# Kernel tuning notes

Measured on AMD Instinct MI355X. Metric: run time of the kernel, lower is better.

Reference implementation:

```python
import jax, jax.numpy as jnp
import numpy as np

N_NODES = 50000
N_EDGES = 800000
C_IN = 128
C_OUT = 64
C_HID = 2 * C_OUT  # 128


def setup_inputs() -> dict:
    key = jax.random.key(0)
    ks = jax.random.split(key, 8)
    x = jax.random.normal(ks[0], (N_NODES, C_IN), dtype=jnp.float32)
    edge_index = jax.random.randint(ks[1], (2, N_EDGES), 0, N_NODES, dtype=jnp.int64)
    s1 = 1.0 / np.sqrt(C_IN)
    s2 = 1.0 / np.sqrt(C_HID)
    s3 = 1.0 / np.sqrt(C_OUT)
    W1 = jax.random.uniform(ks[2], (C_IN, C_HID), jnp.float32, -s1, s1)
    b1 = jnp.zeros((C_HID,), jnp.float32)
    W2 = jax.random.uniform(ks[3], (C_HID, C_OUT), jnp.float32, -s2, s2)
    b2 = jnp.zeros((C_OUT,), jnp.float32)
    Wb = jax.random.uniform(ks[4], (1, C_OUT, C_OUT), jnp.float32, -s3, s3)
    bb = jax.random.uniform(ks[5], (1,), jnp.float32, -s3, s3)
    return {"x": x, "edge_index": edge_index, "W1": W1, "b1": b1,
            "W2": W2, "b2": b2, "Wb": Wb, "bb": bb}


def gcn_conv(x, W, b, src, dst, n_nodes):
    # PyG GCNConv: h = x @ W; add self-loops; symmetric normalization D^-1/2 (A+I) D^-1/2.
    h = x @ W  # [N, F]
    ones = jnp.ones((src.shape[0],), h.dtype)
    deg = jax.ops.segment_sum(ones, dst, num_segments=n_nodes) + 1.0  # +1 for self-loop
    dinv = jax.lax.rsqrt(deg)
    norm = dinv[src] * dinv[dst]  # [E]
    msgs = h[src] * norm[:, None]  # [E, F]
    agg = jax.ops.segment_sum(msgs, dst, num_segments=n_nodes)
    # self-loop contribution: norm_ii = 1/deg_i
    agg = agg + h * (1.0 / deg)[:, None]
    return agg + b


def reference(x, edge_index, W1, b1, W2, b2, Wb, bb):
    src = edge_index[0]
    dst = edge_index[1]
    n = x.shape[0]
    # encode
    h = jax.nn.relu(gcn_conv(x, W1, b1, src, dst, n))
    z = gcn_conv(h, W2, b2, src, dst, n)  # [N, C_OUT]
    # decode: bilinear on (z[src], z[dst]) -> sigmoid
    zs = z[src]  # [E, C_OUT]
    zd = z[dst]  # [E, C_OUT]
    logits = jnp.einsum('ec,ocd,ed->eo', zs, Wb, zd) + bb  # [E, 1]
    return jax.nn.sigmoid(logits)
```

## Files before the change

### kernel.cpp

```cpp
#include <hip/hip_runtime.h>
#include <hip/hip_bf16.h>


#define N_NODES 50000
#define BSH 7
#define BSZ 128
#define NBUCK ((N_NODES + BSZ - 1) / BSZ)
#define EPB 4096
#define CAP 3072
#define DSPLIT 4

typedef unsigned int u32;
typedef unsigned short u16;
typedef unsigned long long u64;

typedef __attribute__((ext_vector_type(8))) short bf16x8;
typedef __attribute__((ext_vector_type(4))) float f32x4;
union frag_u { bf16x8 f; u32 u[4]; uint4 v; };

__device__ __forceinline__ float bflo(u32 u) { return __uint_as_float(u << 16); }
__device__ __forceinline__ float bfhi(u32 u) { return __uint_as_float(u & 0xffff0000u); }
__device__ __forceinline__ u32 f2bf(float f) {
    u32 b = __float_as_uint(f);
    return (b + 0x7fffu + ((b >> 16) & 1u)) >> 16;
}
__device__ __forceinline__ u32 pack2(float a, float b) { return f2bf(a) | (f2bf(b) << 16); }

__global__ __launch_bounds__(256) void gemm1_scatter(
        const float* __restrict__ X, const float* __restrict__ W,
        u16* __restrict__ O, int n_rows, int gblk,
        const int* __restrict__ src, const int* __restrict__ dst,
        int* __restrict__ bcur, u64* __restrict__ pair, int E) {
    constexpr int K = 128, NOUT = 128;
    constexpr int KP = K + 8;
    constexpr int NT = NOUT / 16;
    constexpr int KS = K / 32;
    __shared__ __align__(16) char smem[NOUT * KP * 2 * sizeof(u16)];
    int t = threadIdx.x;

    if ((int)blockIdx.x < gblk) {
        u16* Wt_hi = (u16*)smem;
        u16* Wt_lo = Wt_hi + NOUT * KP;
        for (int i4 = t; i4 < K * NOUT / 4; i4 += 256) {
            int k = (i4 * 4) / NOUT;
            int n0 = (i4 * 4) % NOUT;
            float4 w4 = *(const float4*)&W[(size_t)k * NOUT + n0];
            float wv[4] = {w4.x, w4.y, w4.z, w4.w};
#pragma unroll
            for (int q = 0; q < 4; q++) {
                u32 hi = f2bf(wv[q]);
                u32 lo = f2bf(wv[q] - bflo(hi));
                Wt_hi[(n0 + q) * KP + k] = (u16)hi;
                Wt_lo[(n0 + q) * KP + k] = (u16)lo;
            }
        }
        __syncthreads();

        int wave = t >> 6;
        int lane = t & 63;
        int m16 = lane & 15;
        int quad = lane >> 4;
        int row0 = blockIdx.x * 128 + wave * 32;

        f32x4 acc[2][NT] = {};
        for (int ks = 0; ks < KS; ks++) {
            frag_u a_hi[2], a_lo[2];
#pragma unroll
            for (int mt = 0; mt < 2; mt++) {
                int row = row0 + mt * 16 + m16;
                row = row < n_rows ? row : n_rows - 1;
                const float* Xp = X + (size_t)row * K + ks * 32 + quad * 8;
                float4 x0 = *(const float4*)Xp;
                float4 x1 = *(const float4*)(Xp + 4);
                float xv[8] = {x0.x, x0.y, x0.z, x0.w, x1.x, x1.y, x1.z, x1.w};
#pragma unroll
                for (int p = 0; p < 4; p++) {
                    u32 h0 = f2bf(xv[2 * p]), h1 = f2bf(xv[2 * p + 1]);
                    a_hi[mt].u[p] = h0 | (h1 << 16);
                    a_lo[mt].u[p] = pack2(xv[2 * p] - bflo(h0), xv[2 * p + 1] - bflo(h1));
                }
            }
#pragma unroll
            for (int nt = 0; nt < NT; nt++) {
                int n = nt * 16 + m16;
                frag_u b_hi, b_lo;
                b_hi.v = *(const uint4*)&Wt_hi[n * KP + ks * 32 + quad * 8];
                b_lo.v = *(const uint4*)&Wt_lo[n * KP + ks * 32 + quad * 8];
#pragma unroll
                for (int mt = 0; mt < 2; mt++) {
                    acc[mt][nt] = __builtin_amdgcn_mfma_f32_16x16x32_bf16(a_hi[mt].f, b_hi.f, acc[mt][nt], 0, 0, 0);
                    acc[mt][nt] = __builtin_amdgcn_mfma_f32_16x16x32_bf16(a_hi[mt].f, b_lo.f, acc[mt][nt], 0, 0, 0);
                    acc[mt][nt] = __builtin_amdgcn_mfma_f32_16x16x32_bf16(a_lo[mt].f, b_hi.f, acc[mt][nt], 0, 0, 0);
                }
            }
        }
#pragma unroll
        for (int mt = 0; mt < 2; mt++)
#pragma unroll
            for (int nt = 0; nt < NT; nt++)
#pragma unroll
                for (int r = 0; r < 4; r++) {
                    int row = row0 + mt * 16 + quad * 4 + r;
                    if (row < n_rows)
                        O[(size_t)row * NOUT + nt * 16 + m16] = (u16)f2bf(acc[mt][nt][r]);
                }
    } else {
        int* hist = (int*)smem;
        for (int i = t; i < NBUCK; i += 256) hist[i] = 0;
        __syncthreads();
        int base = ((int)blockIdx.x - gblk) * EPB;
        int s_[16], d_[16];
#pragma unroll
        for (int it = 0; it < 16; it++) {
            int e = base + it * 256 + t;
            if (e < E) {
                s_[it] = src[e];
                d_[it] = dst[e];
                atomicAdd(&hist[d_[it] >> BSH], 1);
            } else {
                d_[it] = -1;
            }
        }
        __syncthreads();
        for (int b = t; b < NBUCK; b += 256) {
            int c = hist[b];
            hist[b] = c ? (b * CAP + atomicAdd(&bcur[b], c)) : 0;
        }
        __syncthreads();
#pragma unroll
        for (int it = 0; it < 16; it++) {
            if (d_[it] >= 0) {
                int b = d_[it] >> BSH;
                int off = atomicAdd(&hist[b], 1);
                int e = base + it * 256 + t;
                pair[off] = (u64)((u32)s_[it] | ((u32)(d_[it] & (BSZ - 1)) << 16))
                          | ((u64)(u32)e << 32);
            }
        }
    }
}

__global__ __launch_bounds__(256) void bucket_sort(const u64* __restrict__ pair,
                                                   const int* __restrict__ bcur,
                                                   int* __restrict__ row_ptr,
                                                   int* __restrict__ col,
                                                   u32* __restrict__ eidx,
                                                   float* __restrict__ dinv,
                                                   float* __restrict__ inv, int n, int E) {
    __shared__ int ssum[256];
    __shared__ int cnt[BSZ];
    __shared__ int scn[BSZ];
    __shared__ int cur[BSZ];
    int t = threadIdx.x;
    int base = blockIdx.x << BSH;
    int nn = min(BSZ, n - base);
    int accp = 0;
    for (int i = t; i < (int)blockIdx.x; i += 256) accp += bcur[i];
    ssum[t] = accp;
    __syncthreads();
    for (int s = 128; s > 0; s >>= 1) {
        if (t < s) ssum[t] += ssum[t + s];
        __syncthreads();
    }
    int b0 = ssum[0];
    int cntE = bcur[blockIdx.x];
    int p0 = blockIdx.x * CAP;
    if (t < BSZ) cnt[t] = 0;
    __syncthreads();
    for (int j = t; j < cntE; j += 256)
        atomicAdd(&cnt[(int)((pair[p0 + j] >> 16) & (BSZ - 1))], 1);
    __syncthreads();
    if (t < BSZ) scn[t] = cnt[t];
    __syncthreads();
    for (int off = 1; off < BSZ; off <<= 1) {
        int a = (t < BSZ && t >= off) ? scn[t - off] : 0;
        __syncthreads();
        if (t < BSZ) scn[t] += a;
        __syncthreads();
    }
    if (t < nn) {
        int excl = b0 + scn[t] - cnt[t];
        row_ptr[base + t] = excl;
        cur[t] = excl;
        float d = (float)cnt[t] + 1.0f;
        dinv[base + t] = rsqrtf(d);
        inv[base + t] = 1.0f / d;
    }
    if (t == 0 && blockIdx.x == NBUCK - 1) row_ptr[n] = E;
    __syncthreads();
    for (int j = t; j < cntE; j += 256) {
        u64 p = pair[p0 + j];
        int ln = (int)((p >> 16) & (BSZ - 1));
        int pos = atomicAdd(&cur[ln], 1);
        col[pos] = (int)(p & 0xffffu);
        eidx[pos] = (u32)(p >> 32) | ((u32)ln << 20);
    }
}

template <int K, int NOUT, bool TRANSW>
__global__ __launch_bounds__(256) void gemm_mfma_bf(const u16* __restrict__ Xv,
                                                    const float* __restrict__ W,
                                                    u16* __restrict__ O, int n_rows) {
    constexpr int KP = K + 8;
    constexpr int NT = NOUT / 16;
    constexpr int KS = K / 32;
    __shared__ __align__(16) u16 Wt_hi[NOUT * KP];
    __shared__ __align__(16) u16 Wt_lo[NOUT * KP];
    int t = threadIdx.x;
    for (int i4 = t; i4 < K * NOUT / 4; i4 += 256) {
        if constexpr (!TRANSW) {
            int k = (i4 * 4) / NOUT;
            int n0 = (i4 * 4) % NOUT;
            float4 w4 = *(const float4*)&W[(size_t)k * NOUT + n0];
            float wv[4] = {w4.x, w4.y, w4.z, w4.w};
#pragma unroll
            for (int q = 0; q < 4; q++) {
                u32 hi = f2bf(wv[q]);
                u32 lo = f2bf(wv[q] - bflo(hi));
                Wt_hi[(n0 + q) * KP + k] = (u16)hi;
                Wt_lo[(n0 + q) * KP + k] = (u16)lo;
            }
        } else {
            int n = (i4 * 4) / K;
            int k0 = (i4 * 4) % K;
            float4 w4 = *(const float4*)&W[(size_t)n * K + k0];
            float wv[4] = {w4.x, w4.y, w4.z, w4.w};
#pragma unroll
            for (int q = 0; q < 4; q++) {
                u32 hi = f2bf(wv[q]);
                u32 lo = f2bf(wv[q] - bflo(hi));
                Wt_hi[n * KP + k0 + q] = (u16)hi;
                Wt_lo[n * KP + k0 + q] = (u16)lo;
            }
        }
    }
    __syncthreads();

    int wave = t >> 6;
    int lane = t & 63;
    int m16 = lane & 15;
    int quad = lane >> 4;
    int row0 = blockIdx.x * 128 + wave * 32;

    f32x4 acc[2][NT] = {};
    for (int ks = 0; ks < KS; ks++) {
        frag_u a_hi[2];
#pragma unroll
        for (int mt = 0; mt < 2; mt++) {
            int row = row0 + mt * 16 + m16;
            row = row < n_rows ? row : n_rows - 1;
            a_hi[mt].v = *(const uint4*)(Xv + (size_t)row * K + ks * 32 + quad * 8);
        }
#pragma unroll
        for (int nt = 0; nt < NT; nt++) {
            int n = nt * 16 + m16;
            frag_u b_hi, b_lo;
            b_hi.v = *(const uint4*)&Wt_hi[n * KP + ks * 32 + quad * 8];
            b_lo.v = *(const uint4*)&Wt_lo[n * KP + ks * 32 + quad * 8];
#pragma unroll
            for (int mt = 0; mt < 2; mt++) {
                acc[mt][nt] = __builtin_amdgcn_mfma_f32_16x16x32_bf16(a_hi[mt].f, b_hi.f, acc[mt][nt], 0, 0, 0);
                acc[mt][nt] = __builtin_amdgcn_mfma_f32_16x16x32_bf16(a_hi[mt].f, b_lo.f, acc[mt][nt], 0, 0, 0);
            }
        }
    }
#pragma unroll
    for (int mt = 0; mt < 2; mt++)
#pragma unroll
        for (int nt = 0; nt < NT; nt++)
#pragma unroll
            for (int r = 0; r < 4; r++) {
                int row = row0 + mt * 16 + quad * 4 + r;
                if (row < n_rows)
                    O[(size_t)row * NOUT + nt * 16 + m16] = (u16)f2bf(acc[mt][nt][r]);
            }
}

template <int C, bool RELU>
__global__ __launch_bounds__(256) void agg_pull(const u16* __restrict__ H,
                                                const int* __restrict__ row_ptr,
                                                const int* __restrict__ col,
                                                const float* __restrict__ dinv,
                                                const float* __restrict__ inv,
                                                const float* __restrict__ b,
                                                u16* __restrict__ O, int n) {
    constexpr int TPN = C / 8;
    const uint4* Hv = (const uint4*)H;
    int tid = blockIdx.x * 256 + threadIdx.x;
    int node = tid / TPN;
    if (node >= n) return;
    int part = tid % TPN;
    int c8 = part * 8;
    float dn = dinv[node];
    float iv = inv[node];
    float acc[8];
    {
        uint4 h = Hv[(size_t)node * TPN + part];
        acc[0] = bflo(h.x) * iv + b[c8 + 0];
        acc[1] = bfhi(h.x) * iv + b[c8 + 1];
        acc[2] = bflo(h.y) * iv + b[c8 + 2];
        acc[3] = bfhi(h.y) * iv + b[c8 + 3];
        acc[4] = bflo(h.z) * iv + b[c8 + 4];
        acc[5] = bfhi(h.z) * iv + b[c8 + 5];
        acc[6] = bflo(h.w) * iv + b[c8 + 6];
        acc[7] = bfhi(h.w) * iv + b[c8 + 7];
    }
    int j = row_ptr[node];
    int end = row_ptr[node + 1];
    for (; j + 3 < end; j += 4) {
        int s0 = col[j], s1 = col[j + 1], s2 = col[j + 2], s3 = col[j + 3];
        float n0 = dn * dinv[s0], n1 = dn * dinv[s1];
        float n2 = dn * dinv[s2], n3 = dn * dinv[s3];
        uint4 v0 = Hv[(size_t)s0 * TPN + part];
        uint4 v1 = Hv[(size_t)s1 * TPN + part];
        uint4 v2 = Hv[(size_t)s2 * TPN + part];
        uint4 v3 = Hv[(size_t)s3 * TPN + part];
        acc[0] += bflo(v0.x) * n0 + bflo(v1.x) * n1 + bflo(v2.x) * n2 + bflo(v3.x) * n3;
        acc[1] += bfhi(v0.x) * n0 + bfhi(v1.x) * n1 + bfhi(v2.x) * n2 + bfhi(v3.x) * n3;
        acc[2] += bflo(v0.y) * n0 + bflo(v1.y) * n1 + bflo(v2.y) * n2 + bflo(v3.y) * n3;
        acc[3] += bfhi(v0.y) * n0 + bfhi(v1.y) * n1 + bfhi(v2.y) * n2 + bfhi(v3.y) * n3;
        acc[4] += bflo(v0.z) * n0 + bflo(v1.z) * n1 + bflo(v2.z) * n2 + bflo(v3.z) * n3;
        acc[5] += bfhi(v0.z) * n0 + bfhi(v1.z) * n1 + bfhi(v2.z) * n2 + bfhi(v3.z) * n3;
        acc[6] += bflo(v0.w) * n0 + bflo(v1.w) * n1 + bflo(v2.w) * n2 + bflo(v3.w) * n3;
        acc[7] += bfhi(v0.w) * n0 + bfhi(v1.w) * n1 + bfhi(v2.w) * n2 + bfhi(v3.w) * n3;
    }
    for (; j < end; j++) {
        int s = col[j];
        float nm = dn * dinv[s];
        uint4 v = Hv[(size_t)s * TPN + part];
        acc[0] += bflo(v.x) * nm; acc[1] += bfhi(v.x) * nm;
        acc[2] += bflo(v.y) * nm; acc[3] += bfhi(v.y) * nm;
        acc[4] += bflo(v.z) * nm; acc[5] += bfhi(v.z) * nm;
        acc[6] += bflo(v.w) * nm; acc[7] += bfhi(v.w) * nm;
    }
    if (RELU) {
#pragma unroll
        for (int i = 0; i < 8; i++) acc[i] = fmaxf(acc[i], 0.f);
    }
    uint4 o;
    o.x = pack2(acc[0], acc[1]);
    o.y = pack2(acc[2], acc[3]);
    o.z = pack2(acc[4], acc[5]);
    o.w = pack2(acc[6], acc[7]);
    ((uint4*)O)[(size_t)node * TPN + part] = o;
}

__global__ __launch_bounds__(256) void decode_csr(const u16* __restrict__ Z,
                                                  const u16* __restrict__ Q,
                                                  const int* __restrict__ row_ptr,
                                                  const int* __restrict__ col,
                                                  const u32* __restrict__ eidx,
                                                  const float* __restrict__ bb,
                                                  float* __restrict__ out, int n) {
    const uint4* Zv = (const uint4*)Z;
    const uint4* Qv = (const uint4*)Q;
    int bucket = blockIdx.x / DSPLIT;
    int part = blockIdx.x % DSPLIT;
    int base = bucket << BSH;
    int nn = min(BSZ, n - base);
    int j0 = row_ptr[base];
    int j1 = row_ptr[base + nn];
    int cnt = j1 - j0;
    int chunk = (cnt + DSPLIT - 1) / DSPLIT;
    int s0 = j0 + part * chunk;
    int s1 = min(s0 + chunk, j1);
    float bbv = bb[0];
    int lane = threadIdx.x & 7;
    for (int j = s0 + ((int)threadIdx.x >> 3); j < s1; j += 32) {
        int s = col[j];
        u32 m = eidx[j];
        int loc = (int)(m >> 20);
        int eid = (int)(m & 0xfffffu);
        uint4 z = Zv[(size_t)s * 8 + lane];
        uint4 q = Qv[(size_t)(base + loc) * 8 + lane];
        float p = bflo(z.x) * bflo(q.x) + bfhi(z.x) * bfhi(q.x)
                + bflo(z.y) * bflo(q.y) + bfhi(z.y) * bfhi(q.y)
                + bflo(z.z) * bflo(q.z) + bfhi(z.z) * bfhi(q.z)
                + bflo(z.w) * bflo(q.w) + bfhi(z.w) * bfhi(q.w);
        p += __shfl_down(p, 4, 8);
        p += __shfl_down(p, 2, 8);
        p += __shfl_down(p, 1, 8);
        if (lane == 0) out[eid] = 1.0f / (1.0f + expf(-(p + bbv)));
    }
}

extern "C" void kernel_launch(void* const* d_in, const int* in_sizes, int n_in,
                              void* d_out, int out_size, void* d_ws, size_t ws_size,
                              hipStream_t stream) {
    const float* x  = (const float*)d_in[0];
    const int*   ei = (const int*)d_in[1];
    const float* W1 = (const float*)d_in[2];
    const float* b1 = (const float*)d_in[3];
    const float* W2 = (const float*)d_in[4];
    const float* b2 = (const float*)d_in[5];
    const float* Wb = (const float*)d_in[6];
    const float* bb = (const float*)d_in[7];
    float* out = (float*)d_out;

    const int N = N_NODES;
    const int E = in_sizes[1] / 2;
    const int* src = ei;
    const int* dst = ei + E;
    const int GBLK = (N + 127) / 128;
    const int SBLK = (E + EPB - 1) / EPB;

    char* w = (char*)d_ws;
    int*   bcur    = (int*)w;   w += (size_t)512 * 4;
    int*   row_ptr = (int*)w;   w += (size_t)(N + 1) * 4;
    int*   col     = (int*)w;   w += (size_t)E * 4;
    u32*   eidx    = (u32*)w;   w += (size_t)E * 4;
    w = (char*)(((size_t)w + 15) & ~(size_t)15);
    u64*   pair    = (u64*)w;   w += (size_t)NBUCK * CAP * 8;
    float* dinv    = (float*)w; w += (size_t)N * 4;
    float* inv     = (float*)w; w += (size_t)N * 4;
    w = (char*)(((size_t)w + 15) & ~(size_t)15);
    u16* bufA = (u16*)w;        w += (size_t)N * 128 * 2;
    u16* bufB = (u16*)w;        w += (size_t)N * 128 * 2;
    u16* bufC = (u16*)w;

    u16* H1 = bufA;
    u16* h1 = bufB;
    u16* H2 = bufA;
    u16* Z  = bufC;
    u16* Q  = bufA + (size_t)N * 64;

    hipMemsetAsync(bcur, 0, 512 * 4, stream);
    gemm1_scatter<<<GBLK + SBLK, 256, 0, stream>>>(x, W1, H1, N, GBLK,
                                                   src, dst, bcur, pair, E);
    bucket_sort<<<NBUCK, 256, 0, stream>>>(pair, bcur, row_ptr, col, eidx, dinv, inv, N, E);

    agg_pull<128, true><<<((size_t)N * 16 + 255) / 256, 256, 0, stream>>>(
        H1, row_ptr, col, dinv, inv, b1, h1, N);

    gemm_mfma_bf<128, 64, false><<<GBLK, 256, 0, stream>>>(h1, W2, H2, N);
    agg_pull<64, false><<<((size_t)N * 8 + 255) / 256, 256, 0, stream>>>(
        H2, row_ptr, col, dinv, inv, b2, Z, N);

    gemm_mfma_bf<64, 64, true><<<GBLK, 256, 0, stream>>>(Z, Wb, Q, N);
    decode_csr<<<NBUCK * DSPLIT, 256, 0, stream>>>(Z, Q, row_ptr, col, eidx, bb, out, N);
}
```

Before: 236.0 us.

## Fuse Q=Z·Wb GEMM into decode kernel and read bucketed pairs directly

Removes the separate Z·Wb GEMM launch and computes each bucket's 128-row Q tile in shared memory inside the decode kernel, using MFMA with a hi/lo bf16 split of Wb. The decode now reads edges straight from the bucketed pair array instead of the CSR col/eidx arrays, so bucket_sort no longer writes eidx. This saves one kernel launch, the global Q write and read, and the eidx stores. The cost is that each of the DSPLIT blocks per bucket recomputes the same Q tile, and the pair array is read unsorted within each bucket.

New measurement: 232.4 us. No clear change (-1.5%).

```diff
diff --git a/kernel.cpp b/kernel.cpp
--- a/kernel.cpp
+++ b/kernel.cpp
@@ -144,7 +144,6 @@
                                                    const int* __restrict__ bcur,
                                                    int* __restrict__ row_ptr,
                                                    int* __restrict__ col,
-                                                   u32* __restrict__ eidx,
                                                    float* __restrict__ dinv,
                                                    float* __restrict__ inv, int n, int E) {
     __shared__ int ssum[256];
@@ -193,11 +192,10 @@
         int ln = (int)((p >> 16) & (BSZ - 1));
         int pos = atomicAdd(&cur[ln], 1);
         col[pos] = (int)(p & 0xffffu);
-        eidx[pos] = (u32)(p >> 32) | ((u32)ln << 20);
-    }
-}
-
-template <int K, int NOUT, bool TRANSW>
+    }
+}
+
+template <int K, int NOUT>
 __global__ __launch_bounds__(256) void gemm_mfma_bf(const u16* __restrict__ Xv,
                                                     const float* __restrict__ W,
                                                     u16* __restrict__ O, int n_rows) {
@@ -208,30 +206,16 @@
     __shared__ __align__(16) u16 Wt_lo[NOUT * KP];
     int t = threadIdx.x;
     for (int i4 = t; i4 < K * NOUT / 4; i4 += 256) {
-        if constexpr (!TRANSW) {
-            int k = (i4 * 4) / NOUT;
-            int n0 = (i4 * 4) % NOUT;
-            float4 w4 = *(const float4*)&W[(size_t)k * NOUT + n0];
-            float wv[4] = {w4.x, w4.y, w4.z, w4.w};
-#pragma unroll
-            for (int q = 0; q < 4; q++) {
-                u32 hi = f2bf(wv[q]);
-                u32 lo = f2bf(wv[q] - bflo(hi));
-                Wt_hi[(n0 + q) * KP + k] = (u16)hi;
-                Wt_lo[(n0 + q) * KP + k] = (u16)lo;
-            }
-        } else {
-            int n = (i4 * 4) / K;
-            int k0 = (i4 * 4) % K;
-            float4 w4 = *(const float4*)&W[(size_t)n * K + k0];
-            float wv[4] = {w4.x, w4.y, w4.z, w4.w};
-#pragma unroll
-            for (int q = 0; q < 4; q++) {
-                u32 hi = f2bf(wv[q]);
-                u32 lo = f2bf(wv[q] - bflo(hi));
-                Wt_hi[n * KP + k0 + q] = (u16)hi;
-                Wt_lo[n * KP + k0 + q] = (u16)lo;
-            }
+        int k = (i4 * 4) / NOUT;
+        int n0 = (i4 * 4) % NOUT;
+        float4 w4 = *(const float4*)&W[(size_t)k * NOUT + n0];
+        float wv[4] = {w4.x, w4.y, w4.z, w4.w};
+#pragma unroll
+        for (int q = 0; q < 4; q++) {
+            u32 hi = f2bf(wv[q]);
+            u32 lo = f2bf(wv[q] - bflo(hi));
+            Wt_hi[(n0 + q) * KP + k] = (u16)hi;
+            Wt_lo[(n0 + q) * KP + k] = (u16)lo;
         }
     }
     __syncthreads();
@@ -345,42 +329,101 @@
     ((uint4*)O)[(size_t)node * TPN + part] = o;
 }
 
-__global__ __launch_bounds__(256) void decode_csr(const u16* __restrict__ Z,
-                                                  const u16* __restrict__ Q,
-                                                  const int* __restrict__ row_ptr,
-                                                  const int* __restrict__ col,
-                                                  const u32* __restrict__ eidx,
-                                                  const float* __restrict__ bb,
-                                                  float* __restrict__ out, int n) {
-    const uint4* Zv = (const uint4*)Z;
-    const uint4* Qv = (const uint4*)Q;
+__global__ __launch_bounds__(256) void decode_fused(const u16* __restrict__ Z,
+                                                    const float* __restrict__ Wb,
+                                                    const u64* __restrict__ pair,
+                                                    const int* __restrict__ bcur,
+                                                    const float* __restrict__ bb,
+                                                    float* __restrict__ out, int n) {
+    constexpr int K = 64, NOUT = 64;
+    constexpr int KP = K + 8;
+    constexpr int QP = 72;
+    __shared__ __align__(16) u16 Wt_hi[NOUT * KP];
+    __shared__ __align__(16) u16 Wt_lo[NOUT * KP];
+    __shared__ __align__(16) u16 Qs[BSZ * QP];
+    int t = threadIdx.x;
     int bucket = blockIdx.x / DSPLIT;
     int part = blockIdx.x % DSPLIT;
     int base = bucket << BSH;
-    int nn = min(BSZ, n - base);
-    int j0 = row_ptr[base];
-    int j1 = row_ptr[base + nn];
-    int cnt = j1 - j0;
-    int chunk = (cnt + DSPLIT - 1) / DSPLIT;
-    int s0 = j0 + part * chunk;
-    int s1 = min(s0 + chunk, j1);
+
+    for (int i4 = t; i4 < K * NOUT / 4; i4 += 256) {
+        int nn_ = (i4 * 4) / K;
+        int k0 = (i4 * 4) % K;
+        float4 w4 = *(const float4*)&Wb[(size_t)nn_ * K + k0];
+        float wv[4] = {w4.x, w4.y, w4.z, w4.w};
+#pragma unroll
+        for (int q = 0; q < 4; q++) {
+            u32 hi = f2bf(wv[q]);
+            u32 lo = f2bf(wv[q] - bflo(hi));
+            Wt_hi[nn_ * KP + k0 + q] = (u16)hi;
+            Wt_lo[nn_ * KP + k0 + q] = (u16)lo;
+        }
+    }
+    __syncthreads();
+
+    {
+        int wave = t >> 6;
+        int lane = t & 63;
+        int m16 = lane & 15;
+        int quad = lane >> 4;
+        int row0 = wave * 32;
+        f32x4 acc[2][4] = {};
+        for (int ks = 0; ks < 2; ks++) {
+            frag_u a[2];
+#pragma unroll
+            for (int mt = 0; mt < 2; mt++) {
+                int node = base + row0 + mt * 16 + m16;
+                node = node < n ? node : n - 1;
+                a[mt].v = *(const uint4*)(Z + (size_t)node * K + ks * 32 + quad * 8);
+            }
+#pragma unroll
+            for (int nt = 0; nt < 4; nt++) {
+                int nc = nt * 16 + m16;
+                frag_u b_hi, b_lo;
+                b_hi.v = *(const uint4*)&Wt_hi[nc * KP + ks * 32 + quad * 8];
+                b_lo.v = *(const uint4*)&Wt_lo[nc * KP + ks * 32 + quad * 8];
+#pragma unroll
+                for (int mt = 0; mt < 2; mt++) {
+                    acc[mt][nt] = __builtin_amdgcn_mfma_f32_16x16x32_bf16(a[mt].f, b_hi.f, acc[mt][nt], 0, 0, 0);
+                    acc[mt][nt] = __builtin_amdgcn_mfma_f32_16x16x32_bf16(a[mt].f, b_lo.f, acc[mt][nt], 0, 0, 0);
+                }
+            }
+        }
+#pragma unroll
+        for (int mt = 0; mt < 2; mt++)
+#pragma unroll
+            for (int nt = 0; nt < 4; nt++)
+#pragma unroll
+                for (int r = 0; r < 4; r++) {
+                    int rl = row0 + mt * 16 + quad * 4 + r;
+                    Qs[rl * QP + nt * 16 + m16] = (u16)f2bf(acc[mt][nt][r]);
+                }
+    }
+    __syncthreads();
+
+    const uint4* Zv = (const uint4*)Z;
+    int cntE = bcur[bucket];
+    int p0 = bucket * CAP;
+    int chunk = (cntE + DSPLIT - 1) / DSPLIT;
+    int s0 = part * chunk;
+    int s1 = min(s0 + chunk, cntE);
     float bbv = bb[0];
-    int lane = threadIdx.x & 7;
-    for (int j = s0 + ((int)threadIdx.x >> 3); j < s1; j += 32) {
-        int s = col[j];
-        u32 m = eidx[j];
-        int loc = (int)(m >> 20);
-        int eid = (int)(m & 0xfffffu);
-        uint4 z = Zv[(size_t)s * 8 + lane];
-        uint4 q = Qv[(size_t)(base + loc) * 8 + lane];
-        float p = bflo(z.x) * bflo(q.x) + bfhi(z.x) * bfhi(q.x)
-                + bflo(z.y) * bflo(q.y) + bfhi(z.y) * bfhi(q.y)
-                + bflo(z.z) * bflo(q.z) + bfhi(z.z) * bfhi(q.z)
-                + bflo(z.w) * bflo(q.w) + bfhi(z.w) * bfhi(q.w);
-        p += __shfl_down(p, 4, 8);
-        p += __shfl_down(p, 2, 8);
-        p += __shfl_down(p, 1, 8);
-        if (lane == 0) out[eid] = 1.0f / (1.0f + expf(-(p + bbv)));
+    int lane8 = t & 7;
+    for (int j = s0 + (t >> 3); j < s1; j += 32) {
+        u64 p = pair[p0 + j];
+        int s = (int)(p & 0xffffu);
+        int loc = (int)((p >> 16) & (BSZ - 1));
+        int eid = (int)(p >> 32);
+        uint4 z = Zv[(size_t)s * 8 + lane8];
+        uint4 q = *(const uint4*)&Qs[loc * QP + lane8 * 8];
+        float pd = bflo(z.x) * bflo(q.x) + bfhi(z.x) * bfhi(q.x)
+                 + bflo(z.y) * bflo(q.y) + bfhi(z.y) * bfhi(q.y)
+                 + bflo(z.z) * bflo(q.z) + bfhi(z.z) * bfhi(q.z)
+                 + bflo(z.w) * bflo(q.w) + bfhi(z.w) * bfhi(q.w);
+        pd += __shfl_down(pd, 4, 8);
+        pd += __shfl_down(pd, 2, 8);
+        pd += __shfl_down(pd, 1, 8);
+        if (lane8 == 0) out[eid] = 1.0f / (1.0f + expf(-(pd + bbv)));
     }
 }
 
@@ -408,7 +451,6 @@
     int*   bcur    = (int*)w;   w += (size_t)512 * 4;
     int*   row_ptr = (int*)w;   w += (size_t)(N + 1) * 4;
     int*   col     = (int*)w;   w += (size_t)E * 4;
-    u32*   eidx    = (u32*)w;   w += (size_t)E * 4;
     w = (char*)(((size_t)w + 15) & ~(size_t)15);
     u64*   pair    = (u64*)w;   w += (size_t)NBUCK * CAP * 8;
     float* dinv    = (float*)w; w += (size_t)N * 4;
@@ -422,20 +464,18 @@
     u16* h1 = bufB;
     u16* H2 = bufA;
     u16* Z  = bufC;
-    u16* Q  = bufA + (size_t)N * 64;
 
     hipMemsetAsync(bcur, 0, 512 * 4, stream);
     gemm1_scatter<<<GBLK + SBLK, 256, 0, stream>>>(x, W1, H1, N, GBLK,
                                                    src, dst, bcur, pair, E);
-    bucket_sort<<<NBUCK, 256, 0, stream>>>(pair, bcur, row_ptr, col, eidx, dinv, inv, N, E);
+    bucket_sort<<<NBUCK, 256, 0, stream>>>(pair, bcur, row_ptr, col, dinv, inv, N, E);
 
     agg_pull<128, true><<<((size_t)N * 16 + 255) / 256, 256, 0, stream>>>(
         H1, row_ptr, col, dinv, inv, b1, h1, N);
 
-    gemm_mfma_bf<128, 64, false><<<GBLK, 256, 0, stream>>>(h1, W2, H2, N);
+    gemm_mfma_bf<128, 64><<<GBLK, 256, 0, stream>>>(h1, W2, H2, N);
     agg_pull<64, false><<<((size_t)N * 8 + 255) / 256, 256, 0, stream>>>(
         H2, row_ptr, col, dinv, inv, b2, Z, N);
 
-    gemm_mfma_bf<64, 64, true><<<GBLK, 256, 0, stream>>>(Z, Wb, Q, N);
-    decode_csr<<<NBUCK * DSPLIT, 256, 0, stream>>>(Z, Q, row_ptr, col, eidx, bb, out, N);
-}
+    decode_fused<<<NBUCK * DSPLIT, 256, 0, stream>>>(Z, Wb, pair, bcur, bb, out, N);
+}
```
